# Kernel optimization log

Measured on AMD Instinct MI355X. Metric: run time of the kernel, lower is better.

The kernel has to match this reference:

```python
import jax, jax.numpy as jnp
import numpy as np

# cfg constants (init_kwargs)
NMS_THRESH = 0.6
CONF_THRESH = 0.05
TOPN = 1000           # nms_thresh_topN: pre-NMS cap and post-NMS cap
NUM_CLASSES = 80
CLS_OFFSET = 4096.0   # > max image coord; class-aware NMS via coordinate offset


def setup_inputs() -> dict:
    key = jax.random.key(0)
    k0, k1, k2, k3 = jax.random.split(key, 4)
    B, H, W, C = 16, 128, 128, NUM_CLASSES
    N = H * W
    image_h, image_w = 1024, 1024
    # anchor-point pixel coordinates for this FPN level
    locations = jax.random.uniform(k0, (N, 2), dtype=jnp.float32) * 1024.0
    pred_cls = jax.random.normal(k1, (B, H, W, C), dtype=jnp.float32)
    # (l, t, r, b) distances are positive
    pred_boxes = jax.random.uniform(k2, (B, H, W, 4), dtype=jnp.float32) * 64.0
    pred_centerness = jax.random.normal(k3, (B, H, W), dtype=jnp.float32)
    return {"locations": locations, "pred_cls": pred_cls, "pred_boxes": pred_boxes,
            "pred_centerness": pred_centerness, "image_h": image_h, "image_w": image_w}


def _pairwise_iou(b):  # b: [K, 4] xyxy
    x1, y1, x2, y2 = b[:, 0], b[:, 1], b[:, 2], b[:, 3]
    area = jnp.maximum(x2 - x1, 0.0) * jnp.maximum(y2 - y1, 0.0)
    ix1 = jnp.maximum(x1[:, None], x1[None, :])
    iy1 = jnp.maximum(y1[:, None], y1[None, :])
    ix2 = jnp.minimum(x2[:, None], x2[None, :])
    iy2 = jnp.minimum(y2[:, None], y2[None, :])
    inter = jnp.maximum(ix2 - ix1, 0.0) * jnp.maximum(iy2 - iy1, 0.0)
    return inter / (area[:, None] + area[None, :] - inter + 1e-9)


def _nms_keep(iou, valid):
    # greedy NMS over score-descending candidates; iou: [B,K,K], valid: [B,K] bool
    K = iou.shape[-1]
    ar = jnp.arange(K)

    def body(i, keep):
        iou_i = jax.lax.dynamic_index_in_dim(iou, i, axis=1, keepdims=False)  # [B,K]
        keep_i = jnp.take(keep, i, axis=1)                                    # [B]
        sup = (iou_i > NMS_THRESH) & (ar[None, :] > i) & keep_i[:, None]
        return keep & ~sup

    return jax.lax.fori_loop(0, K, body, valid)


def reference(locations, pred_cls, pred_boxes, pred_centerness, image_h, image_w):
    B, H, W, C = pred_cls.shape
    N = H * W
    cls = jax.nn.sigmoid(pred_cls.reshape(B, N, C))
    ctr = jax.nn.sigmoid(pred_centerness.reshape(B, N))
    boxes = pred_boxes.reshape(B, N, 4)
    scores = cls * ctr[:, :, None]                    # [B,N,C]
    mask = cls > CONF_THRESH
    neg = jnp.asarray(-jnp.inf, scores.dtype)
    flat = jnp.where(mask, scores, neg).reshape(B, N * C)
    # pre-NMS top-K over masked (location, class) candidates; emulates
    # cls_mask_top_n = clamp(mask.sum(), max=topN) + topk in the torch code
    vals, idx = jax.lax.top_k(flat, TOPN)             # [B,K]
    valid = jnp.isfinite(vals)
    loc_i = idx // C                                  # location index
    lab = idx % C + 1                                 # 1-based class label
    pb = jnp.take_along_axis(boxes, loc_i[:, :, None], axis=1)   # [B,K,4] (l,t,r,b)
    locs = locations[loc_i]                                       # [B,K,2]
    x1 = jnp.clip(locs[..., 0] - pb[..., 0], 0.0, image_w - 1)
    y1 = jnp.clip(locs[..., 1] - pb[..., 1], 0.0, image_h - 1)
    x2 = jnp.clip(locs[..., 0] + pb[..., 2], 0.0, image_w - 1)
    y2 = jnp.clip(locs[..., 1] + pb[..., 3], 0.0, image_h - 1)
    det = jnp.stack([x1, y1, x2, y2], axis=-1)        # [B,K,4] xyxy, clipped
    score = jnp.where(valid, vals, 0.0)
    # sort by score descending for greedy NMS
    order = jnp.argsort(-score, axis=1)
    score = jnp.take_along_axis(score, order, axis=1)
    valid = jnp.take_along_axis(valid, order, axis=1)
    lab = jnp.take_along_axis(lab, order, axis=1)
    det = jnp.take_along_axis(det, order[:, :, None], axis=1)
    # per-class NMS via class-offset trick (boxes of different classes never overlap)
    iou = jax.vmap(_pairwise_iou)(det + lab.astype(det.dtype)[:, :, None] * CLS_OFFSET)
    keep = _nms_keep(iou, valid) & valid
    # final topN (nms_thresh_topN) is a no-op here: candidates <= TOPN already
    boxes_out = det * keep[:, :, None].astype(det.dtype)
    scores_out = jnp.where(keep, score, 0.0)
    labels_out = jnp.where(keep, lab, 0)
    return boxes_out, scores_out, labels_out
```

## Files before the change

### kernel.cpp

```cpp
#include <hip/hip_runtime.h>

#define B_    16
#define N_    16384
#define C_    80
#define NC_   (N_ * C_)
#define TOPN_ 1000
#define T0_   0.70f
#define T0KEY_ 0x3F333333u
#define RKEY_  0x3E800000u
#define NBIN_  4096
#define BLKCAP_ 512
#define RESCCAP_ 8192

#define OFF_CNT    0u
#define OFF_CAND   16384u
#define OFF_RESC   (16384u + 16777216u)

__device__ __forceinline__ float sigm(float x) { return 1.0f / (1.0f + expf(-x)); }

__device__ __forceinline__ int binof(unsigned key) {
    int b = (int)((key - RKEY_) >> 12);
    return b > (NBIN_ - 1) ? (NBIN_ - 1) : b;
}
__device__ __forceinline__ unsigned key_lb(int b) {
    return RKEY_ + ((unsigned)b << 12);
}

__global__ __launch_bounds__(256, 4) void k_pass1(const float* __restrict__ cls,
                                                  const float* __restrict__ ctr,
                                                  unsigned* __restrict__ cnt,
                                                  unsigned long long* __restrict__ cand) {
    __shared__ float xh[64];
    __shared__ float sbv[64];
    __shared__ unsigned long long stage[BLKCAP_];
    __shared__ unsigned lcnt;
    const int blk = blockIdx.x, t = threadIdx.x;
    const int b = blk >> 8, k = blk & 255;
    if (t == 0) lcnt = 0;
    if (t < 64) {
        float sc = sigm(ctr[b * N_ + k * 64 + t]);
        sbv[t] = sc;
        float q = T0_ / sc;
        xh[t] = (q < 1.f) ? (logf(q / (1.f - q)) - 1e-3f) : 3.0e38f;
    }
    __syncthreads();
    const float4* p = (const float4*)(cls + (size_t)b * NC_ + (size_t)k * 5120);
    float4 v[5];
    #pragma unroll
    for (int i = 0; i < 5; ++i) v[i] = p[5 * t + i];
    const int r = t >> 2;
    const float thr = xh[r];
    float mx = v[0].x;
    #pragma unroll
    for (int i = 0; i < 5; ++i)
        mx = fmaxf(mx, fmaxf(fmaxf(v[i].x, v[i].y), fmaxf(v[i].z, v[i].w)));
    if (mx >= thr) {
        const float sb = sbv[r];
        #pragma unroll
        for (int i = 0; i < 5; ++i) {
            float xs[4] = {v[i].x, v[i].y, v[i].z, v[i].w};
            #pragma unroll
            for (int j = 0; j < 4; ++j) {
                if (xs[j] >= thr) {
                    float sapx = sb * __builtin_amdgcn_rcpf(1.f + __expf(-xs[j]));
                    if (sapx >= T0_ * 0.999f) {
                        float s = sigm(xs[j]);
                        unsigned key = __float_as_uint(s * sb);
                        if (key >= T0KEY_) {
                            unsigned pos = atomicAdd(&lcnt, 1u);
                            if (pos < (unsigned)BLKCAP_) {
                                unsigned e = (unsigned)(k * 5120 + (5 * t + i) * 4 + j);
                                stage[pos] = ((unsigned long long)key << 32) |
                                             (unsigned long long)(0xFFFFFFFFu - e);
                            }
                        }
                    }
                }
            }
        }
    }
    __syncthreads();
    unsigned lc = lcnt; if (lc > (unsigned)BLKCAP_) lc = (unsigned)BLKCAP_;
    if (t == 0) cnt[blk] = lc;
    unsigned long long* seg = cand + ((size_t)blk << 9);
    for (unsigned i = t; i < lc; i += 256) seg[i] = stage[i];
}

union TailSMem {
    struct {
        unsigned hbin[NBIN_];
        unsigned binBase[NBIN_];
        unsigned long long srt[2048];
        unsigned long long srt2[1024];
    } s;
    struct {
        float4 bxo[1024];
        unsigned short clsList[1024];
        unsigned clsStart[81];
        unsigned clsCur[81];
        unsigned short supIdx[1024 * 16];
        unsigned char nsup[1024];
    } c;
};

__global__ __launch_bounds__(1024) void k_tail(
        const unsigned long long* __restrict__ cand, const unsigned* __restrict__ cnt,
        unsigned long long* __restrict__ resc,
        const float* __restrict__ boxes, const float* __restrict__ locs,
        const int* __restrict__ ph, const int* __restrict__ pw,
        const float* __restrict__ cls, const float* __restrict__ ctr,
        float* __restrict__ out) {
    __shared__ TailSMem u;
    __shared__ unsigned csh[256];
    __shared__ unsigned Lsh, totSh, rcnt, rcwSh;
    __shared__ unsigned long long keepw[16];
    __shared__ unsigned long long vmaskSh[16];
    const int b = blockIdx.x, t = threadIdx.x;
    const int wv = t >> 6, lane = t & 63;

    if (t == 0) { rcnt = 0; rcwSh = 0; }
    if (t < 256) {
        unsigned cc = cnt[b * 256 + t];
        csh[t] = cc > (unsigned)BLKCAP_ ? (unsigned)BLKCAP_ : cc;
    }
    __syncthreads();
    if (t < 64) {
        unsigned s4 = csh[4 * t] + csh[4 * t + 1] + csh[4 * t + 2] + csh[4 * t + 3];
        #pragma unroll
        for (int off = 32; off >= 1; off >>= 1) s4 += __shfl_down(s4, off, 64);
        if (t == 0) totSh = s4;
    }
    __syncthreads();
    if (totSh < (unsigned)TOPN_) {
        unsigned long long* rs = resc + ((size_t)b << 13);
        const float4* p = (const float4*)(cls + (size_t)b * NC_);
        for (unsigned f = t; f < (unsigned)(NC_ / 4); f += 1024) {
            float4 v = p[f];
            unsigned nl = f / 20;
            float sb = sigm(ctr[b * N_ + nl]);
            float xs[4] = {v.x, v.y, v.z, v.w};
            #pragma unroll
            for (int j = 0; j < 4; ++j) {
                float s = sigm(xs[j]);
                if (s > 0.05f) {
                    unsigned key = __float_as_uint(s * sb);
                    if (key >= RKEY_ && key < T0KEY_) {
                        unsigned pos = atomicAdd(&rcnt, 1u);
                        if (pos < (unsigned)RESCCAP_) {
                            unsigned e = 4u * f + (unsigned)j;
                            rs[pos] = ((unsigned long long)key << 32) |
                                      (unsigned long long)(0xFFFFFFFFu - e);
                        }
                    }
                }
            }
        }
        __syncthreads();
        if (t == 0) {
            unsigned rc = rcnt;
            rcwSh = rc > (unsigned)RESCCAP_ ? (unsigned)RESCCAP_ : rc;
        }
        __syncthreads();
    }

    #pragma unroll
    for (int i = 0; i < 4; ++i) u.s.hbin[t + 1024 * i] = 0;
    u.s.srt[t] = 0ull; u.s.srt[t + 1024] = 0ull;
    u.s.srt2[t] = 0ull;
    __syncthreads();
    const unsigned long long* g = cand + ((size_t)b << 17);
    const unsigned long long* rs = resc + ((size_t)b << 13);
    const unsigned rcw = rcwSh;
    for (int si = 0; si < 16; ++si) {
        int s = wv * 16 + si;
        unsigned cc = csh[s];
        const unsigned long long* gs = g + ((size_t)s << 9);
        for (unsigned o = lane; o < cc; o += 64)
            atomicAdd(&u.s.hbin[binof((unsigned)(gs[o] >> 32))], 1u);
    }
    for (unsigned o = t; o < rcw; o += 1024)
        atomicAdd(&u.s.hbin[binof((unsigned)(rs[o] >> 32))], 1u);
    __syncthreads();
    if (t < 64) {
        const int l = t;
        unsigned cs = 0;
        for (int i = 0; i < 64; ++i) cs += u.s.hbin[64 * l + i];
        unsigned S = cs;
        #pragma unroll
        for (int off = 1; off < 64; off <<= 1) {
            unsigned y = __shfl_down(S, off, 64);
            if (l + off < 64) S += y;
        }
        unsigned acc = S - cs;
        int bc_l = NBIN_;
        for (int b2 = 63; b2 >= 0; --b2) {
            int bin = 64 * l + b2;
            u.s.binBase[bin] = acc;
            if (acc < (unsigned)TOPN_) bc_l = bin;
            acc += u.s.hbin[bin];
        }
        #pragma unroll
        for (int off = 1; off < 64; off <<= 1) {
            int y = __shfl_down(bc_l, off, 64);
            bc_l = bc_l < y ? bc_l : y;
        }
        if (l == 0) Lsh = key_lb(bc_l < NBIN_ ? bc_l : 0);
    }
    __syncthreads();
    const unsigned Lk = Lsh;
    for (int si = 0; si < 16; ++si) {
        int s = wv * 16 + si;
        unsigned cc = csh[s];
        const unsigned long long* gs = g + ((size_t)s << 9);
        for (unsigned o = lane; o < cc; o += 64) {
            unsigned long long comp = gs[o];
            unsigned key = (unsigned)(comp >> 32);
            if (key >= Lk) {
                unsigned slot = atomicAdd(&u.s.binBase[binof(key)], 1u);
                if (slot < 2048u) u.s.srt[slot] = comp;
            }
        }
    }
    for (unsigned o = t; o < rcw; o += 1024) {
        unsigned long long comp = rs[o];
        unsigned key = (unsigned)(comp >> 32);
        if (key >= Lk) {
            unsigned slot = atomicAdd(&u.s.binBase[binof(key)], 1u);
            if (slot < 2048u) u.s.srt[slot] = comp;
        }
    }
    __syncthreads();
    #pragma unroll
    for (int pp = 0; pp < 2; ++pp) {
        unsigned p = (unsigned)t + 1024u * pp;
        unsigned long long comp = u.s.srt[p];
        if (comp) {
            int bin = binof((unsigned)(comp >> 32));
            unsigned endq = u.s.binBase[bin];
            unsigned pop = u.s.hbin[bin];
            unsigned beg = endq - pop;
            unsigned end2 = endq > 2048u ? 2048u : endq;
            unsigned rank = 0;
            for (unsigned j = beg; j < end2; ++j) rank += (u.s.srt[j] > comp);
            unsigned pos = beg + rank;
            if (pos < 1024u) u.s.srt2[pos] = comp;
        }
    }
    __syncthreads();
    unsigned long long comp = u.s.srt2[t];
    unsigned key = (unsigned)(comp >> 32);
    float4 d = {0.f, 0.f, 0.f, 0.f}, doff = {0.f, 0.f, 0.f, 0.f};
    float sc = 0.f; int lb = 0;
    if (key) {
        unsigned idx = 0xFFFFFFFFu - (unsigned)comp;
        unsigned loc = idx / (unsigned)C_;
        unsigned cc2 = idx - loc * (unsigned)C_;
        lb = (int)cc2 + 1;
        float4 pb = ((const float4*)boxes)[(size_t)b * N_ + loc];
        float lx = locs[2 * loc], ly = locs[2 * loc + 1];
        float Wm1 = (float)(pw[0] - 1), Hm1 = (float)(ph[0] - 1);
        d.x = fminf(fmaxf(lx - pb.x, 0.f), Wm1);
        d.y = fminf(fmaxf(ly - pb.y, 0.f), Hm1);
        d.z = fminf(fmaxf(lx + pb.z, 0.f), Wm1);
        d.w = fminf(fmaxf(ly + pb.w, 0.f), Hm1);
        sc = __uint_as_float(key);
        float off = (float)lb * 4096.0f;
        doff.x = d.x + off; doff.y = d.y + off; doff.z = d.z + off; doff.w = d.w + off;
    }
    const bool valid = (key != 0u);
    {
        unsigned long long ball = __ballot(valid);
        if ((t & 63) == 0) vmaskSh[t >> 6] = ball;
    }
    __syncthreads();

    u.c.bxo[t] = doff;
    if (t < 81) u.c.clsStart[t] = 0;
    __syncthreads();
    if (lb > 0) atomicAdd(&u.c.clsStart[lb], 1u);
    __syncthreads();
    if (t < 64) {
        const int l = t;
        unsigned s0 = 0, s1 = 0;
        if (l < 40) { s0 = u.c.clsStart[2 * l + 1]; s1 = u.c.clsStart[2 * l + 2]; }
        unsigned p = s0 + s1;
        unsigned S = p;
        #pragma unroll
        for (int off = 1; off < 64; off <<= 1) {
            unsigned y = __shfl_up(S, off, 64);
            if (l >= off) S += y;
        }
        unsigned excl = S - p;
        if (l < 40) {
            u.c.clsStart[2 * l + 1] = excl;
            u.c.clsCur[2 * l + 1]   = excl;
            u.c.clsStart[2 * l + 2] = excl + s0;
            u.c.clsCur[2 * l + 2]   = excl + s0;
        }
    }
    __syncthreads();
    if (lb > 0) {
        unsigned pos = atomicAdd(&u.c.clsCur[lb], 1u);
        u.c.clsList[pos] = (unsigned short)t;
    }
    __syncthreads();
    unsigned nsup = 0;
    if (valid) {
        float4 A = doff;
        float aA = fmaxf(A.z - A.x, 0.f) * fmaxf(A.w - A.y, 0.f);
        unsigned beg = u.c.clsStart[lb], end = u.c.clsCur[lb];
        for (unsigned q = beg; q < end; ++q) {
            int j = (int)u.c.clsList[q];
            if (j < t) {
                float4 Bv = u.c.bxo[j];
                float aB = fmaxf(Bv.z - Bv.x, 0.f) * fmaxf(Bv.w - Bv.y, 0.f);
                float ix1 = fmaxf(A.x, Bv.x), iy1 = fmaxf(A.y, Bv.y);
                float ix2 = fminf(A.z, Bv.z), iy2 = fminf(A.w, Bv.w);
                float inter = fmaxf(ix2 - ix1, 0.f) * fmaxf(iy2 - iy1, 0.f);
                float iou = inter / (aA + aB - inter + 1e-9f);
                if (iou > 0.6f) {
                    if (nsup < 16u) u.c.supIdx[t * 16 + nsup] = (unsigned short)j;
                    ++nsup;
                }
            }
        }
        if (nsup > 16u) nsup = 16u;
    }
    u.c.nsup[t] = (unsigned char)nsup;
    __syncthreads();

    if (t < 64) {
        const int ii = t;
        for (int gg = 0; gg < 16; ++gg) {
            const int row = gg * 64 + ii;
            const unsigned base = (unsigned)(gg << 6);
            unsigned ns = u.c.nsup[row];
            unsigned long long diag = 0;
            bool supP = false;
            for (unsigned q = 0; q < ns; ++q) {
                unsigned j = (unsigned)u.c.supIdx[row * 16 + q];
                if (j < base) {
                    if ((keepw[j >> 6] >> (j & 63)) & 1ull) supP = true;
                } else {
                    diag |= 1ull << (j & 63);
                }
            }
            bool alive = (((vmaskSh[gg] >> ii) & 1ull) != 0) && !supP;
            unsigned long long undec = __ballot(alive);
            unsigned long long kept = 0;
            while (undec) {
                bool meU = ((undec >> ii) & 1ull) != 0;
                bool supK = (kept & diag) != 0;
                bool anyU = (undec & diag) != 0;
                unsigned long long bkm = __ballot(meU && !supK && !anyU);
                unsigned long long brm = __ballot(meU && supK);
                kept |= bkm;
                undec &= ~(bkm | brm);
            }
            if (ii == 0) keepw[gg] = kept;
        }
    }
    __syncthreads();

    if (t < TOPN_) {
        bool kp = ((keepw[t >> 6] >> (t & 63)) & 1ull) != 0;
        ((float4*)out)[(size_t)b * TOPN_ + t] = kp ? d : make_float4(0.f, 0.f, 0.f, 0.f);
        out[B_ * TOPN_ * 4 + b * TOPN_ + t] = kp ? sc : 0.f;
        out[B_ * TOPN_ * 5 + b * TOPN_ + t] = kp ? (float)lb : 0.f;
    }
}

extern "C" void kernel_launch(void* const* d_in, const int* in_sizes, int n_in,
                              void* d_out, int out_size, void* d_ws, size_t ws_size,
                              hipStream_t stream) {
    (void)in_sizes; (void)n_in; (void)out_size; (void)ws_size;
    const float* locations = (const float*)d_in[0];
    const float* pred_cls  = (const float*)d_in[1];
    const float* pred_box  = (const float*)d_in[2];
    const float* pred_ctr  = (const float*)d_in[3];
    const int*   ph        = (const int*)d_in[4];
    const int*   pw        = (const int*)d_in[5];
    float* out = (float*)d_out;

    char* w = (char*)d_ws;
    unsigned* cnt            = (unsigned*)(w + OFF_CNT);
    unsigned long long* cand = (unsigned long long*)(w + OFF_CAND);
    unsigned long long* resc = (unsigned long long*)(w + OFF_RESC);


    k_pass1<<<4096, 256, 0, stream>>>(pred_cls, pred_ctr, cnt, cand);
    k_tail<<<B_, 1024, 0, stream>>>(cand, cnt, resc, pred_box, locations, ph, pw,
                                    pred_cls, pred_ctr, out);
}
```

Measured before the change: 169.4 us.

## Precompute clipped boxes in pass1 and gather by slot index in tail

Pass1 now loads the per-row box distances and locations into shared memory and stores the decoded, clipped box alongside each candidate key in a 32-byte record. The tail tracks a slot index through the sort and fetches the precomputed box from that record, so only rescue-path candidates still gather boxes and locations from global memory. The per-block candidate cap drops to 128, and the histogram and scatter loops now assign four threads to each segment. The goal is to move the scattered box gathers off the serial single-block-per-image tail and into the parallel pass, at the cost of more pass1 work and a risk of overflowing the smaller cap.

```diff
diff --git a/kernel.cpp b/kernel.cpp
--- a/kernel.cpp
+++ b/kernel.cpp
@@ -9,8 +9,10 @@
 #define T0KEY_ 0x3F333333u
 #define RKEY_  0x3E800000u
 #define NBIN_  4096
-#define BLKCAP_ 512
+#define BLKCAP_ 128
 #define RESCCAP_ 8192
+
+#define CREC_ 32
 
 #define OFF_CNT    0u
 #define OFF_CAND   16384u
@@ -28,20 +30,32 @@
 
 __global__ __launch_bounds__(256, 4) void k_pass1(const float* __restrict__ cls,
                                                   const float* __restrict__ ctr,
+                                                  const float* __restrict__ boxes,
+                                                  const float* __restrict__ locs,
+                                                  const int* __restrict__ ph,
+                                                  const int* __restrict__ pw,
                                                   unsigned* __restrict__ cnt,
-                                                  unsigned long long* __restrict__ cand) {
+                                                  char* __restrict__ cand) {
     __shared__ float xh[64];
     __shared__ float sbv[64];
-    __shared__ unsigned long long stage[BLKCAP_];
+    __shared__ float lxv[64], lyv[64];
+    __shared__ float4 bxv[64];
+    __shared__ unsigned long long stageC[BLKCAP_];
+    __shared__ float4 stageB[BLKCAP_];
     __shared__ unsigned lcnt;
     const int blk = blockIdx.x, t = threadIdx.x;
     const int b = blk >> 8, k = blk & 255;
     if (t == 0) lcnt = 0;
+    const float Wm1 = (float)(pw[0] - 1), Hm1 = (float)(ph[0] - 1);
     if (t < 64) {
-        float sc = sigm(ctr[b * N_ + k * 64 + t]);
+        int row = k * 64 + t;
+        float sc = sigm(ctr[b * N_ + row]);
         sbv[t] = sc;
         float q = T0_ / sc;
         xh[t] = (q < 1.f) ? (logf(q / (1.f - q)) - 1e-3f) : 3.0e38f;
+        bxv[t] = ((const float4*)boxes)[(size_t)b * N_ + row];
+        lxv[t] = locs[2 * row];
+        lyv[t] = locs[2 * row + 1];
     }
     __syncthreads();
     const float4* p = (const float4*)(cls + (size_t)b * NC_ + (size_t)k * 5120);
@@ -70,8 +84,16 @@
                             unsigned pos = atomicAdd(&lcnt, 1u);
                             if (pos < (unsigned)BLKCAP_) {
                                 unsigned e = (unsigned)(k * 5120 + (5 * t + i) * 4 + j);
-                                stage[pos] = ((unsigned long long)key << 32) |
-                                             (unsigned long long)(0xFFFFFFFFu - e);
+                                stageC[pos] = ((unsigned long long)key << 32) |
+                                              (unsigned long long)(0xFFFFFFFFu - e);
+                                float4 pb = bxv[r];
+                                float lx = lxv[r], ly = lyv[r];
+                                float4 d;
+                                d.x = fminf(fmaxf(lx - pb.x, 0.f), Wm1);
+                                d.y = fminf(fmaxf(ly - pb.y, 0.f), Hm1);
+                                d.z = fminf(fmaxf(lx + pb.z, 0.f), Wm1);
+                                d.w = fminf(fmaxf(ly + pb.w, 0.f), Hm1);
+                                stageB[pos] = d;
                             }
                         }
                     }
@@ -82,8 +104,11 @@
     __syncthreads();
     unsigned lc = lcnt; if (lc > (unsigned)BLKCAP_) lc = (unsigned)BLKCAP_;
     if (t == 0) cnt[blk] = lc;
-    unsigned long long* seg = cand + ((size_t)blk << 9);
-    for (unsigned i = t; i < lc; i += 256) seg[i] = stage[i];
+    char* seg = cand + (size_t)blk * (BLKCAP_ * CREC_);
+    for (unsigned i = t; i < lc; i += 256) {
+        *(unsigned long long*)(seg + (size_t)i * CREC_) = stageC[i];
+        *(float4*)(seg + (size_t)i * CREC_ + 16) = stageB[i];
+    }
 }
 
 union TailSMem {
@@ -91,7 +116,8 @@
         unsigned hbin[NBIN_];
         unsigned binBase[NBIN_];
         unsigned long long srt[2048];
-        unsigned long long srt2[1024];
+        unsigned srtSlot[2048];
+        unsigned srt2Slot[1024];
     } s;
     struct {
         float4 bxo[1024];
@@ -104,7 +130,7 @@
 };
 
 __global__ __launch_bounds__(1024) void k_tail(
-        const unsigned long long* __restrict__ cand, const unsigned* __restrict__ cnt,
+        const char* __restrict__ cand, const unsigned* __restrict__ cnt,
         unsigned long long* __restrict__ resc,
         const float* __restrict__ boxes, const float* __restrict__ locs,
         const int* __restrict__ ph, const int* __restrict__ pw,
@@ -116,7 +142,6 @@
     __shared__ unsigned long long keepw[16];
     __shared__ unsigned long long vmaskSh[16];
     const int b = blockIdx.x, t = threadIdx.x;
-    const int wv = t >> 6, lane = t & 63;
 
     if (t == 0) { rcnt = 0; rcwSh = 0; }
     if (t < 256) {
@@ -132,7 +157,7 @@
     }
     __syncthreads();
     if (totSh < (unsigned)TOPN_) {
-        unsigned long long* rs = resc + ((size_t)b << 13);
+        unsigned long long* rsw = resc + ((size_t)b << 13);
         const float4* p = (const float4*)(cls + (size_t)b * NC_);
         for (unsigned f = t; f < (unsigned)(NC_ / 4); f += 1024) {
             float4 v = p[f];
@@ -148,8 +173,8 @@
                         unsigned pos = atomicAdd(&rcnt, 1u);
                         if (pos < (unsigned)RESCCAP_) {
                             unsigned e = 4u * f + (unsigned)j;
-                            rs[pos] = ((unsigned long long)key << 32) |
-                                      (unsigned long long)(0xFFFFFFFFu - e);
+                            rsw[pos] = ((unsigned long long)key << 32) |
+                                       (unsigned long long)(0xFFFFFFFFu - e);
                         }
                     }
                 }
@@ -166,17 +191,19 @@
     #pragma unroll
     for (int i = 0; i < 4; ++i) u.s.hbin[t + 1024 * i] = 0;
     u.s.srt[t] = 0ull; u.s.srt[t + 1024] = 0ull;
-    u.s.srt2[t] = 0ull;
-    __syncthreads();
-    const unsigned long long* g = cand + ((size_t)b << 17);
+    u.s.srt2Slot[t] = 0xFFFFFFFFu;
+    __syncthreads();
+    const char* gb = cand + ((size_t)b << 20);
     const unsigned long long* rs = resc + ((size_t)b << 13);
     const unsigned rcw = rcwSh;
-    for (int si = 0; si < 16; ++si) {
-        int s = wv * 16 + si;
-        unsigned cc = csh[s];
-        const unsigned long long* gs = g + ((size_t)s << 9);
-        for (unsigned o = lane; o < cc; o += 64)
-            atomicAdd(&u.s.hbin[binof((unsigned)(gs[o] >> 32))], 1u);
+    {
+        const int s = t >> 2;
+        const unsigned cc = csh[s];
+        const char* gs = gb + (size_t)s * (BLKCAP_ * CREC_);
+        for (unsigned o = (unsigned)(t & 3); o < cc; o += 4) {
+            unsigned key = (unsigned)((*(const unsigned long long*)(gs + (size_t)o * CREC_)) >> 32);
+            atomicAdd(&u.s.hbin[binof(key)], 1u);
+        }
     }
     for (unsigned o = t; o < rcw; o += 1024)
         atomicAdd(&u.s.hbin[binof((unsigned)(rs[o] >> 32))], 1u);
@@ -208,16 +235,19 @@
     }
     __syncthreads();
     const unsigned Lk = Lsh;
-    for (int si = 0; si < 16; ++si) {
-        int s = wv * 16 + si;
-        unsigned cc = csh[s];
-        const unsigned long long* gs = g + ((size_t)s << 9);
-        for (unsigned o = lane; o < cc; o += 64) {
-            unsigned long long comp = gs[o];
+    {
+        const int s = t >> 2;
+        const unsigned cc = csh[s];
+        const char* gs = gb + (size_t)s * (BLKCAP_ * CREC_);
+        for (unsigned o = (unsigned)(t & 3); o < cc; o += 4) {
+            unsigned long long comp = *(const unsigned long long*)(gs + (size_t)o * CREC_);
             unsigned key = (unsigned)(comp >> 32);
             if (key >= Lk) {
                 unsigned slot = atomicAdd(&u.s.binBase[binof(key)], 1u);
-                if (slot < 2048u) u.s.srt[slot] = comp;
+                if (slot < 2048u) {
+                    u.s.srt[slot] = comp;
+                    u.s.srtSlot[slot] = (unsigned)(s * BLKCAP_) + o;
+                }
             }
         }
     }
@@ -226,7 +256,10 @@
         unsigned key = (unsigned)(comp >> 32);
         if (key >= Lk) {
             unsigned slot = atomicAdd(&u.s.binBase[binof(key)], 1u);
-            if (slot < 2048u) u.s.srt[slot] = comp;
+            if (slot < 2048u) {
+                u.s.srt[slot] = comp;
+                u.s.srtSlot[slot] = 0x80000000u | o;
+            }
         }
     }
     __syncthreads();
@@ -243,31 +276,41 @@
             unsigned rank = 0;
             for (unsigned j = beg; j < end2; ++j) rank += (u.s.srt[j] > comp);
             unsigned pos = beg + rank;
-            if (pos < 1024u) u.s.srt2[pos] = comp;
-        }
-    }
-    __syncthreads();
-    unsigned long long comp = u.s.srt2[t];
-    unsigned key = (unsigned)(comp >> 32);
+            if (pos < 1024u) u.s.srt2Slot[pos] = u.s.srtSlot[p];
+        }
+    }
+    __syncthreads();
+    unsigned sl = u.s.srt2Slot[t];
     float4 d = {0.f, 0.f, 0.f, 0.f}, doff = {0.f, 0.f, 0.f, 0.f};
     float sc = 0.f; int lb = 0;
-    if (key) {
+    bool valid = (sl != 0xFFFFFFFFu);
+    if (valid) {
+        unsigned long long comp;
+        if (sl & 0x80000000u) {
+            comp = rs[sl & 0x7FFFFFFFu];
+            unsigned idx = 0xFFFFFFFFu - (unsigned)comp;
+            unsigned loc = idx / (unsigned)C_;
+            float4 pb = ((const float4*)boxes)[(size_t)b * N_ + loc];
+            float lx = locs[2 * loc], ly = locs[2 * loc + 1];
+            float Wm1 = (float)(pw[0] - 1), Hm1 = (float)(ph[0] - 1);
+            d.x = fminf(fmaxf(lx - pb.x, 0.f), Wm1);
+            d.y = fminf(fmaxf(ly - pb.y, 0.f), Hm1);
+            d.z = fminf(fmaxf(lx + pb.z, 0.f), Wm1);
+            d.w = fminf(fmaxf(ly + pb.w, 0.f), Hm1);
+        } else {
+            const char* ce = gb + (size_t)sl * CREC_;
+            comp = *(const unsigned long long*)ce;
+            d = *(const float4*)(ce + 16);
+        }
+        unsigned key = (unsigned)(comp >> 32);
         unsigned idx = 0xFFFFFFFFu - (unsigned)comp;
         unsigned loc = idx / (unsigned)C_;
         unsigned cc2 = idx - loc * (unsigned)C_;
         lb = (int)cc2 + 1;
-        float4 pb = ((const float4*)boxes)[(size_t)b * N_ + loc];
-        float lx = locs[2 * loc], ly = locs[2 * loc + 1];
-        float Wm1 = (float)(pw[0] - 1), Hm1 = (float)(ph[0] - 1);
-        d.x = fminf(fmaxf(lx - pb.x, 0.f), Wm1);
-        d.y = fminf(fmaxf(ly - pb.y, 0.f), Hm1);
-        d.z = fminf(fmaxf(lx + pb.z, 0.f), Wm1);
-        d.w = fminf(fmaxf(ly + pb.w, 0.f), Hm1);
         sc = __uint_as_float(key);
         float off = (float)lb * 4096.0f;
         doff.x = d.x + off; doff.y = d.y + off; doff.z = d.z + off; doff.w = d.w + off;
     }
-    const bool valid = (key != 0u);
     {
         unsigned long long ball = __ballot(valid);
         if ((t & 63) == 0) vmaskSh[t >> 6] = ball;
@@ -384,11 +427,12 @@
 
     char* w = (char*)d_ws;
     unsigned* cnt            = (unsigned*)(w + OFF_CNT);
-    unsigned long long* cand = (unsigned long long*)(w + OFF_CAND);
+    char* cand               = (char*)(w + OFF_CAND);
     unsigned long long* resc = (unsigned long long*)(w + OFF_RESC);
 
 
-    k_pass1<<<4096, 256, 0, stream>>>(pred_cls, pred_ctr, cnt, cand);
+    k_pass1<<<4096, 256, 0, stream>>>(pred_cls, pred_ctr, pred_box, locations,
+                                      ph, pw, cnt, cand);
     k_tail<<<B_, 1024, 0, stream>>>(cand, cnt, resc, pred_box, locations, ph, pw,
                                     pred_cls, pred_ctr, out);
 }
```

Result: slower. 174.7 us (+3.1%).
